# Performance work log

Hardware: AMD Instinct MI355X
Metric: run time of the kernel (lower is better)

## Reference

```python
import jax, jax.numpy as jnp
import numpy as np

NEG_SLOPE = 0.01  # F.leaky_relu default

def setup_inputs() -> dict:
    key = jax.random.key(0)
    ks = jax.random.split(key, 5)
    N, in_dim, out_dim = 8192, 256, 256
    x = jax.random.normal(ks[0], (N, in_dim), dtype=jnp.float32)
    W_fc = jax.random.normal(ks[1], (in_dim, out_dim), dtype=jnp.float32) / np.sqrt(in_dim)
    b_fc = jnp.zeros((out_dim,), dtype=jnp.float32)
    # attn_fc weight [2*out_dim] split into the two halves acting on h_i and h_j
    a1 = jax.random.normal(ks[2], (out_dim,), dtype=jnp.float32) / np.sqrt(2 * out_dim)
    a2 = jax.random.normal(ks[3], (out_dim,), dtype=jnp.float32) / np.sqrt(2 * out_dim)
    a_b = jnp.zeros((), dtype=jnp.float32)
    return {"x": x, "W_fc": W_fc, "b_fc": b_fc, "a1": a1, "a2": a2, "a_b": a_b}

def reference(x, W_fc, b_fc, a1, a2, a_b):
    # h = fc(x)
    h = x @ W_fc + b_fc                       # [N, out_dim]
    # attn_fc(cat[h_i, h_j]) == h_i.a1 + h_j.a2 + a_b (exact decomposition of the Linear)
    s1 = h @ a1                               # [N]
    s2 = h @ a2                               # [N]
    e = jax.nn.leaky_relu(s1[:, None] + s2[None, :] + a_b, NEG_SLOPE)  # [N, N]
    attention = jax.nn.softmax(e, axis=1)     # row-softmax over neighbors j
    return attention @ h                      # [N, out_dim]
```

## Files before the change

kernel.cpp:

```cpp
#include <hip/hip_runtime.h>
#include <math.h>


#define NN 8192
#define DD 256
#define NB 8192
#define CH 512
#define POS (NN / CH)
#define RANGE 8.0f
#define SCALE (NB / (2.0f * RANGE))
#define NEG_SLOPE 0.01f

__device__ __forceinline__ int bucket_of(float v) {
    v = fminf(fmaxf(v, -RANGE), RANGE);
    int b = (int)floorf((v + RANGE) * SCALE);
    if (b < 0) b = 0;
    if (b > NB - 1) b = NB - 1;
    return b;
}

__global__ __launch_bounds__(256) void ka_gemm(
    const float* __restrict__ x, const float* __restrict__ W,
    const float* __restrict__ bfc, const float* __restrict__ a1,
    const float* __restrict__ a2,
    float* __restrict__ h, float* __restrict__ s1, float* __restrict__ s2,
    float* __restrict__ E, float* __restrict__ F, int* __restrict__ cnt)
{
    const int d = threadIdx.x;
    const int row0 = blockIdx.x * 16;
    float acc[16];
#pragma unroll
    for (int r = 0; r < 16; ++r) acc[r] = 0.f;

    for (int k4 = 0; k4 < DD / 4; ++k4) {
        const float w0 = W[(4 * k4 + 0) * DD + d];
        const float w1 = W[(4 * k4 + 1) * DD + d];
        const float w2 = W[(4 * k4 + 2) * DD + d];
        const float w3 = W[(4 * k4 + 3) * DD + d];
#pragma unroll
        for (int r = 0; r < 16; ++r) {
            const float4 xv = *reinterpret_cast<const float4*>(&x[(size_t)(row0 + r) * DD + 4 * k4]);
            acc[r] = fmaf(xv.x, w0, fmaf(xv.y, w1, fmaf(xv.z, w2, fmaf(xv.w, w3, acc[r]))));
        }
    }

    const float bb = bfc[d];
    const float a1d = a1[d], a2d = a2[d];
    __shared__ float part1[4][16];
    __shared__ float part2[4][16];
    const int wave = d >> 6, lane = d & 63;

#pragma unroll
    for (int r = 0; r < 16; ++r) {
        acc[r] += bb;
        h[(size_t)(row0 + r) * DD + d] = acc[r];
        float v1 = acc[r] * a1d;
        float v2 = acc[r] * a2d;
#pragma unroll
        for (int off = 32; off; off >>= 1) {
            v1 += __shfl_xor(v1, off, 64);
            v2 += __shfl_xor(v2, off, 64);
        }
        if (lane == 0) { part1[wave][r] = v1; part2[wave][r] = v2; }
    }
    __syncthreads();
    if (d < 32) {
        const int r = d & 15, which = d >> 4;
        if (which == 0) {
            s1[row0 + r] = part1[0][r] + part1[1][r] + part1[2][r] + part1[3][r];
        } else {
            const float s = part2[0][r] + part2[1][r] + part2[2][r] + part2[3][r];
            s2[row0 + r] = s;
            E[row0 + r] = expf(s);
            F[row0 + r] = expf(NEG_SLOPE * s);
            atomicAdd(&cnt[bucket_of(s)], 1);
        }
    }
}

__global__ __launch_bounds__(256) void kb_scan(int* __restrict__ cnt, int* __restrict__ boff)
{
    __shared__ int lds[256];
    const int t = threadIdx.x;
    const int base = t * 32;
    int loc[32];
    int s = 0;
#pragma unroll
    for (int k = 0; k < 32; ++k) { loc[k] = s; s += cnt[base + k]; }
    lds[t] = s;
    __syncthreads();
    for (int off = 1; off < 256; off <<= 1) {
        const int v = (t >= off) ? lds[t - off] : 0;
        __syncthreads();
        lds[t] += v;
        __syncthreads();
    }
    const int excl = (t > 0) ? lds[t - 1] : 0;
#pragma unroll
    for (int k = 0; k < 32; ++k) {
        const int val = excl + loc[k];
        boff[base + k] = val;
        cnt[base + k] = val;
    }
    if (t == 0) boff[NB] = NN;
}

__global__ __launch_bounds__(256) void kc_scatter(
    const float* __restrict__ s2, int* __restrict__ cursor, int* __restrict__ perm)
{
    const int j = blockIdx.x * blockDim.x + threadIdx.x;
    if (j < NN) {
        const int b = bucket_of(s2[j]);
        const int p = atomicAdd(&cursor[b], 1);
        perm[p] = j;
    }
}

__global__ __launch_bounds__(256) void kd1_tot(
    const float* __restrict__ h, const float* __restrict__ E, const float* __restrict__ F,
    const int* __restrict__ perm,
    float* __restrict__ TE, float* __restrict__ TF,
    float* __restrict__ sTE, float* __restrict__ sTF)
{
    const int c = blockIdx.x;
    const int t = threadIdx.x;
    __shared__ int jj[POS];
    __shared__ float Ee[POS], Ff[POS];
    if (t < POS) {
        const int j = perm[c * POS + t];
        jj[t] = j; Ee[t] = E[j]; Ff[t] = F[j];
    }
    __syncthreads();
    float te = 0.f, tf = 0.f;
#pragma unroll
    for (int k = 0; k < POS; ++k) {
        const float hv = h[(size_t)jj[k] * DD + t];
        te = fmaf(Ee[k], hv, te);
        tf = fmaf(Ff[k], hv, tf);
    }
    TE[c * DD + t] = te;
    TF[c * DD + t] = tf;
    if (t == 0) {
        float se = 0.f, sf = 0.f;
#pragma unroll
        for (int k = 0; k < POS; ++k) { se += Ee[k]; sf += Ff[k]; }
        sTE[c] = se; sTF[c] = sf;
    }
}

__global__ __launch_bounds__(512) void kd2_scan(
    float* __restrict__ TE, float* __restrict__ TF,
    float* __restrict__ sTE, float* __restrict__ sTF,
    float* __restrict__ PSE, float* __restrict__ PSF,
    float* __restrict__ psE, float* __restrict__ psF)
{
    const int t = threadIdx.x;
    if (t < 256) {
        float run = 0.f;
        for (int c = CH - 1; c >= 0; --c) { const float v = TE[c * DD + t]; TE[c * DD + t] = run; run += v; }
        PSE[(size_t)NN * DD + t] = 0.f;
    } else {
        const int d = t - 256;
        float run = 0.f;
        for (int c = 0; c < CH; ++c) { const float v = TF[c * DD + d]; TF[c * DD + d] = run; run += v; }
        PSF[(size_t)NN * DD + d] = run;
    }
    __shared__ float a[CH];
    __shared__ float b[CH];
    a[t] = sTE[t];
    b[t] = sTF[t];
    __syncthreads();
    for (int off = 1; off < CH; off <<= 1) {
        const float va = (t + off < CH) ? a[t + off] : 0.f;
        const float vb = (t >= off) ? b[t - off] : 0.f;
        __syncthreads();
        a[t] += va;
        b[t] += vb;
        __syncthreads();
    }
    sTE[t] = (t + 1 < CH) ? a[t + 1] : 0.f;
    sTF[t] = (t > 0) ? b[t - 1] : 0.f;
    if (t == 0) psE[NN] = 0.f;
    if (t == CH - 1) psF[NN] = b[CH - 1];
}

__global__ __launch_bounds__(256) void kd3_write(
    const float* __restrict__ h, const float* __restrict__ E, const float* __restrict__ F,
    const int* __restrict__ perm,
    const float* __restrict__ TE, const float* __restrict__ TF,
    const float* __restrict__ sTE, const float* __restrict__ sTF,
    float* __restrict__ PSE, float* __restrict__ PSF,
    float* __restrict__ psE, float* __restrict__ psF)
{
    const int c = blockIdx.x;
    const int t = threadIdx.x;
    __shared__ int jj[POS];
    __shared__ float Ee[POS], Ff[POS];
    if (t < POS) {
        const int j = perm[c * POS + t];
        jj[t] = j; Ee[t] = E[j]; Ff[t] = F[j];
    }
    __syncthreads();
    const int p0 = c * POS;

    float runE = TE[c * DD + t];
#pragma unroll
    for (int k = POS - 1; k >= 0; --k) {
        runE = fmaf(Ee[k], h[(size_t)jj[k] * DD + t], runE);
        PSE[(size_t)(p0 + k) * DD + t] = runE;
    }
    float runF = TF[c * DD + t];
#pragma unroll
    for (int k = 0; k < POS; ++k) {
        PSF[(size_t)(p0 + k) * DD + t] = runF;
        runF = fmaf(Ff[k], h[(size_t)jj[k] * DD + t], runF);
    }
    if (t == 0) {
        float rE = sTE[c];
#pragma unroll
        for (int k = POS - 1; k >= 0; --k) { rE += Ee[k]; psE[p0 + k] = rE; }
        float rF = sTF[c];
#pragma unroll
        for (int k = 0; k < POS; ++k) { psF[p0 + k] = rF; rF += Ff[k]; }
    }
}

__global__ __launch_bounds__(256) void ke_out(
    const float* __restrict__ h, const float* __restrict__ s1, const float* __restrict__ s2,
    const float* __restrict__ E, const float* __restrict__ F,
    const int* __restrict__ perm, const int* __restrict__ boff,
    const float* __restrict__ PSE, const float* __restrict__ PSF,
    const float* __restrict__ psE, const float* __restrict__ psF,
    const float* __restrict__ ab, float* __restrict__ out)
{
    const int i = blockIdx.x;
    const int t = threadIdx.x;
    const float c = s1[i] + ab[0];
    const float tau = -c;
    const int Bt = bucket_of(tau);
    const float A = expf(c);
    const float Alo = expf(NEG_SLOPE * c);

    const int p0 = boff[Bt], p1 = boff[Bt + 1];
    float num = A * PSE[(size_t)p1 * DD + t] + Alo * PSF[(size_t)p0 * DD + t];
    float den = A * psE[p1] + Alo * psF[p0];

    for (int p = p0; p < p1; ++p) {
        const int j = perm[p];
        const float hv = h[(size_t)j * DD + t];
        if (s2[j] >= tau) {
            const float w = A * E[j];
            num = fmaf(w, hv, num);
            den += w;
        } else {
            const float w = Alo * F[j];
            num = fmaf(w, hv, num);
            den += w;
        }
    }
    out[(size_t)i * DD + t] = num / den;
}

extern "C" void kernel_launch(void* const* d_in, const int* in_sizes, int n_in,
                              void* d_out, int out_size, void* d_ws, size_t ws_size,
                              hipStream_t stream)
{
    const float* x   = (const float*)d_in[0];
    const float* W   = (const float*)d_in[1];
    const float* bfc = (const float*)d_in[2];
    const float* a1  = (const float*)d_in[3];
    const float* a2  = (const float*)d_in[4];
    const float* ab  = (const float*)d_in[5];
    float* out = (float*)d_out;

    float* h   = (float*)d_ws;
    float* PSE = h + (size_t)NN * DD;
    float* PSF = PSE + (size_t)(NN + 1) * DD;
    float* TE  = PSF + (size_t)(NN + 1) * DD;
    float* TF  = TE + (size_t)CH * DD;
    float* s1  = TF + (size_t)CH * DD;
    float* s2  = s1 + NN;
    float* E   = s2 + NN;
    float* F   = E + NN;
    float* psE = F + NN;
    float* psF = psE + (NN + 1);
    float* sTE = psF + (NN + 1);
    float* sTF = sTE + CH;
    int* cnt   = (int*)(sTF + CH);
    int* boff  = cnt + NB;
    int* perm  = boff + (NB + 1);

    hipMemsetAsync(cnt, 0, NB * sizeof(int), stream);
    ka_gemm<<<NN / 16, 256, 0, stream>>>(x, W, bfc, a1, a2, h, s1, s2, E, F, cnt);
    kb_scan<<<1, 256, 0, stream>>>(cnt, boff);
    kc_scatter<<<NN / 256, 256, 0, stream>>>(s2, cnt, perm);
    kd1_tot<<<CH, 256, 0, stream>>>(h, E, F, perm, TE, TF, sTE, sTF);
    kd2_scan<<<1, 512, 0, stream>>>(TE, TF, sTE, sTF, PSE, PSF, psE, psF);
    kd3_write<<<CH, 256, 0, stream>>>(h, E, F, perm, TE, TF, sTE, sTF, PSE, PSF, psE, psF);
    ke_out<<<NN, 256, 0, stream>>>(h, s1, s2, E, F, perm, boff, PSE, PSF, psE, psF, ab, out);
}
```

Before: 173.8 us.

## Register-tile the fc GEMM and parallelize chunk prefix scans across blocks

The fc GEMM now stages the 16 input rows in shared memory and gives each thread a 4x4 register tile with float4 loads of W. Each row's s1/s2 reduction is done by a single wave, which removes the cross-wave shared-memory combine. The single-block serial column scan in kd2_scan is replaced by 513 blocks, each running a parallel LDS scan over one column or over the per-chunk totals. This targets the long serial latency of one block walking 512 chunks for each of 512 columns. In exchange it adds many synchronisations inside each scan and a larger launch.

```diff
diff --git a/kernel.cpp b/kernel.cpp
--- a/kernel.cpp
+++ b/kernel.cpp
@@ -26,54 +26,74 @@
     float* __restrict__ h, float* __restrict__ s1, float* __restrict__ s2,
     float* __restrict__ E, float* __restrict__ F, int* __restrict__ cnt)
 {
-    const int d = threadIdx.x;
+    const int t = threadIdx.x;
+    const int ct = t & 63;
+    const int rt = t >> 6;
     const int row0 = blockIdx.x * 16;
-    float acc[16];
-#pragma unroll
-    for (int r = 0; r < 16; ++r) acc[r] = 0.f;
-
+    __shared__ float xs[16][DD];
+
+#pragma unroll
+    for (int i = 0; i < 4; ++i) {
+        const int f = i * 256 + t;
+        const int r = f >> 6, c4 = f & 63;
+        *reinterpret_cast<float4*>(&xs[r][c4 * 4]) =
+            *reinterpret_cast<const float4*>(&x[(size_t)(row0 + r) * DD + c4 * 4]);
+    }
+    __syncthreads();
+
+    float acc[4][4];
+#pragma unroll
+    for (int r = 0; r < 4; ++r)
+#pragma unroll
+        for (int c = 0; c < 4; ++c) acc[r][c] = 0.f;
+
+#pragma unroll 2
     for (int k4 = 0; k4 < DD / 4; ++k4) {
-        const float w0 = W[(4 * k4 + 0) * DD + d];
-        const float w1 = W[(4 * k4 + 1) * DD + d];
-        const float w2 = W[(4 * k4 + 2) * DD + d];
-        const float w3 = W[(4 * k4 + 3) * DD + d];
-#pragma unroll
-        for (int r = 0; r < 16; ++r) {
-            const float4 xv = *reinterpret_cast<const float4*>(&x[(size_t)(row0 + r) * DD + 4 * k4]);
-            acc[r] = fmaf(xv.x, w0, fmaf(xv.y, w1, fmaf(xv.z, w2, fmaf(xv.w, w3, acc[r]))));
-        }
-    }
-
-    const float bb = bfc[d];
-    const float a1d = a1[d], a2d = a2[d];
-    __shared__ float part1[4][16];
-    __shared__ float part2[4][16];
-    const int wave = d >> 6, lane = d & 63;
-
-#pragma unroll
-    for (int r = 0; r < 16; ++r) {
-        acc[r] += bb;
-        h[(size_t)(row0 + r) * DD + d] = acc[r];
-        float v1 = acc[r] * a1d;
-        float v2 = acc[r] * a2d;
+        float4 wv[4];
+#pragma unroll
+        for (int kk = 0; kk < 4; ++kk)
+            wv[kk] = *reinterpret_cast<const float4*>(&W[(size_t)(k4 * 4 + kk) * DD + ct * 4]);
+        float4 xr[4];
+#pragma unroll
+        for (int r = 0; r < 4; ++r)
+            xr[r] = *reinterpret_cast<const float4*>(&xs[rt * 4 + r][k4 * 4]);
+#pragma unroll
+        for (int kk = 0; kk < 4; ++kk) {
+#pragma unroll
+            for (int r = 0; r < 4; ++r) {
+                const float xv = (kk == 0) ? xr[r].x : (kk == 1) ? xr[r].y : (kk == 2) ? xr[r].z : xr[r].w;
+                acc[r][0] = fmaf(xv, wv[kk].x, acc[r][0]);
+                acc[r][1] = fmaf(xv, wv[kk].y, acc[r][1]);
+                acc[r][2] = fmaf(xv, wv[kk].z, acc[r][2]);
+                acc[r][3] = fmaf(xv, wv[kk].w, acc[r][3]);
+            }
+        }
+    }
+
+    const float4 bv  = *reinterpret_cast<const float4*>(&bfc[ct * 4]);
+    const float4 a1v = *reinterpret_cast<const float4*>(&a1[ct * 4]);
+    const float4 a2v = *reinterpret_cast<const float4*>(&a2[ct * 4]);
+    const int lane = t & 63;
+
+#pragma unroll
+    for (int r = 0; r < 4; ++r) {
+        acc[r][0] += bv.x; acc[r][1] += bv.y; acc[r][2] += bv.z; acc[r][3] += bv.w;
+        const int row = row0 + rt * 4 + r;
+        float4 hv = make_float4(acc[r][0], acc[r][1], acc[r][2], acc[r][3]);
+        *reinterpret_cast<float4*>(&h[(size_t)row * DD + ct * 4]) = hv;
+        float v1 = acc[r][0] * a1v.x + acc[r][1] * a1v.y + acc[r][2] * a1v.z + acc[r][3] * a1v.w;
+        float v2 = acc[r][0] * a2v.x + acc[r][1] * a2v.y + acc[r][2] * a2v.z + acc[r][3] * a2v.w;
 #pragma unroll
         for (int off = 32; off; off >>= 1) {
             v1 += __shfl_xor(v1, off, 64);
             v2 += __shfl_xor(v2, off, 64);
         }
-        if (lane == 0) { part1[wave][r] = v1; part2[wave][r] = v2; }
-    }
-    __syncthreads();
-    if (d < 32) {
-        const int r = d & 15, which = d >> 4;
-        if (which == 0) {
-            s1[row0 + r] = part1[0][r] + part1[1][r] + part1[2][r] + part1[3][r];
-        } else {
-            const float s = part2[0][r] + part2[1][r] + part2[2][r] + part2[3][r];
-            s2[row0 + r] = s;
-            E[row0 + r] = expf(s);
-            F[row0 + r] = expf(NEG_SLOPE * s);
-            atomicAdd(&cnt[bucket_of(s)], 1);
+        if (lane == 0) {
+            s1[row] = v1;
+            s2[row] = v2;
+            E[row] = expf(v2);
+            F[row] = expf(NEG_SLOPE * v2);
+            atomicAdd(&cnt[bucket_of(v2)], 1);
         }
     }
 }
@@ -155,33 +175,57 @@
     float* __restrict__ psE, float* __restrict__ psF)
 {
     const int t = threadIdx.x;
-    if (t < 256) {
-        float run = 0.f;
-        for (int c = CH - 1; c >= 0; --c) { const float v = TE[c * DD + t]; TE[c * DD + t] = run; run += v; }
-        PSE[(size_t)NN * DD + t] = 0.f;
+    const int b = blockIdx.x;
+    __shared__ float lds[CH];
+
+    if (b < 512) {
+        const bool isE = (b < 256);
+        const int d = isE ? b : (b - 256);
+        float* __restrict__ A = isE ? TE : TF;
+        const float v = A[(size_t)t * DD + d];
+        const int pos = isE ? (CH - 1 - t) : t;
+        lds[pos] = v;
+        __syncthreads();
+        for (int off = 1; off < CH; off <<= 1) {
+            const float add = (pos >= off) ? lds[pos - off] : 0.f;
+            __syncthreads();
+            lds[pos] += add;
+            __syncthreads();
+        }
+        const float incl = lds[pos];
+        A[(size_t)t * DD + d] = incl - v;
+        if (t == 0) {
+            if (isE) PSE[(size_t)NN * DD + d] = 0.f;
+            else     PSF[(size_t)NN * DD + d] = lds[CH - 1];
+        }
     } else {
-        const int d = t - 256;
-        float run = 0.f;
-        for (int c = 0; c < CH; ++c) { const float v = TF[c * DD + d]; TF[c * DD + d] = run; run += v; }
-        PSF[(size_t)NN * DD + d] = run;
-    }
-    __shared__ float a[CH];
-    __shared__ float b[CH];
-    a[t] = sTE[t];
-    b[t] = sTF[t];
-    __syncthreads();
-    for (int off = 1; off < CH; off <<= 1) {
-        const float va = (t + off < CH) ? a[t + off] : 0.f;
-        const float vb = (t >= off) ? b[t - off] : 0.f;
-        __syncthreads();
-        a[t] += va;
-        b[t] += vb;
-        __syncthreads();
-    }
-    sTE[t] = (t + 1 < CH) ? a[t + 1] : 0.f;
-    sTF[t] = (t > 0) ? b[t - 1] : 0.f;
-    if (t == 0) psE[NN] = 0.f;
-    if (t == CH - 1) psF[NN] = b[CH - 1];
+        const float vE = sTE[t];
+        const float vF = sTF[t];
+        lds[CH - 1 - t] = vE;
+        __syncthreads();
+        for (int off = 1; off < CH; off <<= 1) {
+            const int pos = CH - 1 - t;
+            const float add = (pos >= off) ? lds[pos - off] : 0.f;
+            __syncthreads();
+            lds[pos] += add;
+            __syncthreads();
+        }
+        const float inclE = lds[CH - 1 - t];
+        __syncthreads();
+        lds[t] = vF;
+        __syncthreads();
+        for (int off = 1; off < CH; off <<= 1) {
+            const float add = (t >= off) ? lds[t - off] : 0.f;
+            __syncthreads();
+            lds[t] += add;
+            __syncthreads();
+        }
+        const float inclF = lds[t];
+        const float totF = lds[CH - 1];
+        sTE[t] = inclE - vE;
+        sTF[t] = inclF - vF;
+        if (t == 0) { psE[NN] = 0.f; psF[NN] = totF; }
+    }
 }
 
 __global__ __launch_bounds__(256) void kd3_write(
@@ -295,7 +339,7 @@
     kb_scan<<<1, 256, 0, stream>>>(cnt, boff);
     kc_scatter<<<NN / 256, 256, 0, stream>>>(s2, cnt, perm);
     kd1_tot<<<CH, 256, 0, stream>>>(h, E, F, perm, TE, TF, sTE, sTF);
-    kd2_scan<<<1, 512, 0, stream>>>(TE, TF, sTE, sTF, PSE, PSF, psE, psF);
+    kd2_scan<<<513, 512, 0, stream>>>(TE, TF, sTE, sTF, PSE, PSF, psE, psF);
     kd3_write<<<CH, 256, 0, stream>>>(h, E, F, perm, TE, TF, sTE, sTF, PSE, PSF, psE, psF);
     ke_out<<<NN, 256, 0, stream>>>(h, s1, s2, E, F, perm, boff, PSE, PSF, psE, psF, ab, out);
 }
```

Result: faster. 144.2 us (-17.0%).
